# Kernel tuning notes

Hardware: AMD Instinct MI355X
Metric: run time of the kernel (lower is better)

The kernel has to match this reference:

```python
import jax, jax.numpy as jnp
import numpy as np

NUM_LEVELS = 16
FEATS_PER_LEVEL = 2
LOG2_HASHMAP = 19
TABLE_SIZE = 1 << LOG2_HASHMAP
BASE_RES = 16
DESIRED_RES = 4096
PER_LEVEL_SCALE = float(np.exp(np.log(DESIRED_RES / BASE_RES) / (NUM_LEVELS - 1)))
PRIMES = (np.uint32(1), np.uint32(2654435761), np.uint32(805459861))
N_POINTS = 2_000_000


def _level_features(x, table, level):
    # x: [N,3] in [0,1]; table: [TABLE_SIZE, F]
    scale = BASE_RES * (PER_LEVEL_SCALE ** level) - 1.0
    res = int(np.ceil(scale)) + 1
    dense = (res ** 3) <= TABLE_SIZE  # tcnn uses dense indexing when grid fits
    pos = x * scale + 0.5
    pos0 = jnp.floor(pos)
    w = pos - pos0                     # trilinear weights, [N,3]
    base = pos0.astype(jnp.uint32)
    out = jnp.zeros((x.shape[0], table.shape[1]), dtype=table.dtype)
    for c in range(8):                 # 8 corners of the voxel
        offs = [(c >> d) & 1 for d in range(3)]
        pc = [jnp.minimum(base[:, d] + np.uint32(offs[d]), np.uint32(res - 1)) for d in range(3)]
        if dense:
            idx = pc[0] + pc[1] * np.uint32(res) + pc[2] * np.uint32(res * res)
        else:
            idx = (pc[0] * PRIMES[0]) ^ (pc[1] * PRIMES[1]) ^ (pc[2] * PRIMES[2])
            idx = idx & np.uint32(TABLE_SIZE - 1)
        wt = jnp.ones(x.shape[0], dtype=x.dtype)
        for d in range(3):
            wt = wt * (w[:, d] if offs[d] else (1.0 - w[:, d]))
        out = out + wt[:, None] * table[idx.astype(jnp.int32)]
    return out


def hashgrid_encode(x, tables):
    # x: [N,3] in [0,1]; tables: [L, TABLE_SIZE, F] -> [N, L*F]
    return jnp.concatenate(
        [_level_features(x, tables[l], l) for l in range(NUM_LEVELS)], axis=-1)


def setup_inputs() -> dict:
    key = jax.random.key(0)
    k1, k2, k3, k4, k5 = jax.random.split(key, 5)
    points = jax.random.uniform(k1, (N_POINTS, 3), dtype=jnp.float32)
    # tcnn hashgrid init: uniform(-1e-4, 1e-4)
    tables = jax.random.uniform(k2, (NUM_LEVELS, TABLE_SIZE, FEATS_PER_LEVEL),
                                minval=-1e-4, maxval=1e-4, dtype=jnp.float32)
    def kaiming(k, fan_out, fan_in):
        bound = np.sqrt(2.0) * np.sqrt(3.0 / fan_in)
        return jax.random.uniform(k, (fan_out, fan_in), minval=-bound, maxval=bound,
                                  dtype=jnp.float32)
    W1 = kaiming(k3, 32, 32)
    W2 = kaiming(k4, 32, 32)
    W3 = kaiming(k5, 4, 32)
    aabb = jnp.stack([jnp.zeros(3, jnp.float32), jnp.ones(3, jnp.float32)])
    return {"points": points, "tables": tables, "W1": W1, "W2": W2, "W3": W3,
            "aabb": aabb}


def reference(points, tables, W1, W2, W3, aabb):
    texc = jnp.clip((points - aabb[0][None, :]) / (aabb[1] - aabb[0])[None, :], 0.0, 1.0)
    enc = hashgrid_encode(texc, tables)            # [N, 32]
    h = jax.nn.relu(enc @ W1.T)
    h = jax.nn.relu(h @ W2.T)
    out = h @ W3.T                                 # [N, 4]
    mn = jnp.array([0.0, 0.0, 0.0, 0.01], dtype=out.dtype)
    mx = jnp.array([1.0, 1.0, 1.0, 1.0], dtype=out.dtype)
    return jax.nn.sigmoid(out) * (mx - mn) + mn
```

## Files before the change

### kernel.cpp

```cpp
#include <hip/hip_runtime.h>
#include <cmath>


namespace {
constexpr int kLevels = 16;
constexpr unsigned kTableSize = 1u << 19;
constexpr unsigned kMask = kTableSize - 1u;
constexpr int kCells = 32768;

typedef _Float16 half2_t __attribute__((ext_vector_type(2)));
typedef unsigned int u32;

struct LevelParams {
  float scale[kLevels];
  unsigned res[kLevels];
  int dense[kLevels];
  unsigned toff[kLevels];
  unsigned cnt[kLevels];
};
}

__global__ __launch_bounds__(256)
void conv_tables_kernel(const float2* __restrict__ src, u32* __restrict__ dst,
                        LevelParams lp,
                        const float* __restrict__ W1, const float* __restrict__ W2,
                        const float* __restrict__ W3, half2_t* __restrict__ Wh)
{
  int gid = blockIdx.x * blockDim.x + threadIdx.x;
  if (gid < 512) {
    Wh[gid] = half2_t{(_Float16)W1[2 * gid], (_Float16)W1[2 * gid + 1]};
  } else if (gid < 1024) {
    int t = gid - 512;
    Wh[512 + t] = half2_t{(_Float16)W2[2 * t], (_Float16)W2[2 * t + 1]};
  } else if (gid < 1088) {
    int t = gid - 1024;
    Wh[1024 + t] = half2_t{(_Float16)W3[2 * t], (_Float16)W3[2 * t + 1]};
  }
  int l = blockIdx.x >> 11;
  unsigned e = (unsigned)((blockIdx.x & 2047) * blockDim.x + threadIdx.x);
  if (l < kLevels && e < lp.cnt[l]) {
    float2 v = src[(size_t)l * kTableSize + e];
    dst[lp.toff[l] + e] =
        __builtin_bit_cast(u32, half2_t{(_Float16)v.x, (_Float16)v.y});
  }
}

__device__ __forceinline__ void texc_of(const float* __restrict__ pts,
                                        const float* __restrict__ aabb, int i,
                                        float& x, float& y, float& z)
{
  float a0x = aabb[0], a0y = aabb[1], a0z = aabb[2];
  float a1x = aabb[3], a1y = aabb[4], a1z = aabb[5];
  x = fminf(fmaxf((pts[3 * i + 0] - a0x) / (a1x - a0x), 0.f), 1.f);
  y = fminf(fmaxf((pts[3 * i + 1] - a0y) / (a1y - a0y), 0.f), 1.f);
  z = fminf(fmaxf((pts[3 * i + 2] - a0z) / (a1z - a0z), 0.f), 1.f);
}

__device__ __forceinline__ int cell_of(float x, float y, float z)
{
  int cx = min((int)(x * 32.f), 31);
  int cy = min((int)(y * 32.f), 31);
  int cz = min((int)(z * 32.f), 31);
  return cx + (cy << 5) + (cz << 10);
}

__global__ __launch_bounds__(256)
void zero_hist_kernel(u32* __restrict__ hist)
{
  int i = blockIdx.x * blockDim.x + threadIdx.x;
  if (i < kCells) hist[i] = 0u;
}

__global__ __launch_bounds__(256)
void hist_kernel(const float* __restrict__ points, const float* __restrict__ aabb,
                 u32* __restrict__ hist, int n)
{
  int i = blockIdx.x * blockDim.x + threadIdx.x;
  if (i >= n) return;
  float x, y, z;
  texc_of(points, aabb, i, x, y, z);
  atomicAdd(&hist[cell_of(x, y, z)], 1u);
}

__global__ __launch_bounds__(1024)
void scan_kernel(u32* __restrict__ hist)
{
  __shared__ u32 sm[1024];
  int t = threadIdx.x;
  u32 loc[32];
  u32 s = 0;
  #pragma unroll
  for (int k = 0; k < 32; ++k) { loc[k] = hist[t * 32 + k]; s += loc[k]; }
  sm[t] = s;
  __syncthreads();
  u32 v = s;
  for (int off = 1; off < 1024; off <<= 1) {
    u32 a = (t >= off) ? sm[t - off] : 0u;
    __syncthreads();
    v += a;
    sm[t] = v;
    __syncthreads();
  }
  u32 run = v - s;
  #pragma unroll
  for (int k = 0; k < 32; ++k) { hist[t * 32 + k] = run; run += loc[k]; }
}

__global__ __launch_bounds__(256)
void scatter_kernel(const float* __restrict__ points, const float* __restrict__ aabb,
                    u32* __restrict__ cstart, float4* __restrict__ sorted,
                    u32* __restrict__ perm, int n)
{
  int i = blockIdx.x * blockDim.x + threadIdx.x;
  if (i >= n) return;
  float x, y, z;
  texc_of(points, aabb, i, x, y, z);
  int c = cell_of(x, y, z);
  u32 slot = atomicAdd(&cstart[c], 1u);
  sorted[slot] = float4{x, y, z, 0.f};
  perm[slot] = (u32)i;
}

__device__ __forceinline__ u32 sel4(uint4 v, u32 j) {
  u32 lo = (j & 1u) ? v.y : v.x;
  u32 hi = (j & 1u) ? v.w : v.z;
  return (j & 2u) ? hi : lo;
}

__global__ __launch_bounds__(256)
void encode_kernel(const float4* __restrict__ pts,
                   const u32* __restrict__ tables,
                   half2_t* __restrict__ enc,
                   LevelParams lp, int n, int bpl)
{
  int l = blockIdx.x / bpl;
  int i = (blockIdx.x - l * bpl) * blockDim.x + threadIdx.x;
  if (i >= n) return;

  float4 p = pts[i];
  float x = p.x, y = p.y, z = p.z;

  float s = lp.scale[l];
  unsigned res = lp.res[l];
  bool dense = (lp.dense[l] != 0);
  unsigned rm1 = res - 1u;
  unsigned res2 = res * res;
  const u32* tab = tables + lp.toff[l];

  float fx = x * s + 0.5f, fy = y * s + 0.5f, fz = z * s + 0.5f;
  float fx0 = floorf(fx), fy0 = floorf(fy), fz0 = floorf(fz);
  float wx = fx - fx0, wy = fy - fy0, wz = fz - fz0;
  unsigned bx = (unsigned)fx0, by = (unsigned)fy0, bz = (unsigned)fz0;

  unsigned pcx0 = min(bx, rm1), pcx1 = min(bx + 1u, rm1);

  u32 idx0[4], idx1[4];
  #pragma unroll
  for (int q = 0; q < 4; ++q) {
    unsigned oy = (unsigned)(q & 1);
    unsigned oz = (unsigned)(q >> 1);
    unsigned pcy = min(by + oy, rm1);
    unsigned pcz = min(bz + oz, rm1);
    if (dense) {
      u32 b = pcy * res + pcz * res2;
      idx0[q] = pcx0 + b;
      idx1[q] = pcx1 + b;
    } else {
      u32 h = (pcy * 2654435761u) ^ (pcz * 805459861u);
      idx0[q] = (pcx0 ^ h) & kMask;
      idx1[q] = (pcx1 ^ h) & kMask;
    }
  }

  uint4 v[4];
  #pragma unroll
  for (int q = 0; q < 4; ++q)
    v[q] = *reinterpret_cast<const uint4*>(tab + (idx0[q] & ~3u));

  u32 e1x[4] = {0u, 0u, 0u, 0u};
  #pragma unroll
  for (int q = 0; q < 4; ++q) {
    if ((idx0[q] ^ idx1[q]) >= 4u) e1x[q] = tab[idx1[q]];
  }

  float wx1 = wx, wx0 = 1.f - wx;
  float acc0 = 0.f, acc1 = 0.f;
  #pragma unroll
  for (int q = 0; q < 4; ++q) {
    unsigned oy = (unsigned)(q & 1);
    unsigned oz = (unsigned)(q >> 1);
    float wyz = (oy ? wy : 1.f - wy) * (oz ? wz : 1.f - wz);
    u32 e0 = sel4(v[q], idx0[q] & 3u);
    u32 e1g = sel4(v[q], idx1[q] & 3u);
    u32 e1 = ((idx0[q] ^ idx1[q]) < 4u) ? e1g : e1x[q];
    half2_t f0 = __builtin_bit_cast(half2_t, e0);
    half2_t f1 = __builtin_bit_cast(half2_t, e1);
    float w0 = wyz * wx0, w1 = wyz * wx1;
    acc0 += w0 * (float)f0.x + w1 * (float)f1.x;
    acc1 += w0 * (float)f0.y + w1 * (float)f1.y;
  }
  enc[(size_t)l * n + i] = half2_t{(_Float16)acc0, (_Float16)acc1};
}

__global__ __launch_bounds__(256)
void encode_raw_kernel(const float* __restrict__ points,
                       const u32* __restrict__ tables,
                       const float* __restrict__ aabb,
                       half2_t* __restrict__ enc,
                       LevelParams lp, int n, int bpl)
{
  int l = blockIdx.x / bpl;
  int i = (blockIdx.x - l * bpl) * blockDim.x + threadIdx.x;
  if (i >= n) return;
  float x, y, z;
  texc_of(points, aabb, i, x, y, z);

  float s = lp.scale[l];
  unsigned res = lp.res[l];
  bool dense = (lp.dense[l] != 0);
  unsigned rm1 = res - 1u;
  unsigned res2 = res * res;
  const u32* tab = tables + lp.toff[l];

  float fx = x * s + 0.5f, fy = y * s + 0.5f, fz = z * s + 0.5f;
  float fx0 = floorf(fx), fy0 = floorf(fy), fz0 = floorf(fz);
  float wx = fx - fx0, wy = fy - fy0, wz = fz - fz0;
  unsigned bx = (unsigned)fx0, by = (unsigned)fy0, bz = (unsigned)fz0;
  unsigned pcx0 = min(bx, rm1), pcx1 = min(bx + 1u, rm1);

  u32 idx0[4], idx1[4];
  #pragma unroll
  for (int q = 0; q < 4; ++q) {
    unsigned oy = (unsigned)(q & 1);
    unsigned oz = (unsigned)(q >> 1);
    unsigned pcy = min(by + oy, rm1);
    unsigned pcz = min(bz + oz, rm1);
    if (dense) {
      u32 b = pcy * res + pcz * res2;
      idx0[q] = pcx0 + b;
      idx1[q] = pcx1 + b;
    } else {
      u32 h = (pcy * 2654435761u) ^ (pcz * 805459861u);
      idx0[q] = (pcx0 ^ h) & kMask;
      idx1[q] = (pcx1 ^ h) & kMask;
    }
  }
  uint4 v[4];
  #pragma unroll
  for (int q = 0; q < 4; ++q)
    v[q] = *reinterpret_cast<const uint4*>(tab + (idx0[q] & ~3u));
  u32 e1x[4] = {0u, 0u, 0u, 0u};
  #pragma unroll
  for (int q = 0; q < 4; ++q) {
    if ((idx0[q] ^ idx1[q]) >= 4u) e1x[q] = tab[idx1[q]];
  }
  float wx1 = wx, wx0 = 1.f - wx;
  float acc0 = 0.f, acc1 = 0.f;
  #pragma unroll
  for (int q = 0; q < 4; ++q) {
    unsigned oy = (unsigned)(q & 1);
    unsigned oz = (unsigned)(q >> 1);
    float wyz = (oy ? wy : 1.f - wy) * (oz ? wz : 1.f - wz);
    u32 e0 = sel4(v[q], idx0[q] & 3u);
    u32 e1g = sel4(v[q], idx1[q] & 3u);
    u32 e1 = ((idx0[q] ^ idx1[q]) < 4u) ? e1g : e1x[q];
    half2_t f0 = __builtin_bit_cast(half2_t, e0);
    half2_t f1 = __builtin_bit_cast(half2_t, e1);
    float w0 = wyz * wx0, w1 = wyz * wx1;
    acc0 += w0 * (float)f0.x + w1 * (float)f1.x;
    acc1 += w0 * (float)f0.y + w1 * (float)f1.y;
  }
  enc[(size_t)l * n + i] = half2_t{(_Float16)acc0, (_Float16)acc1};
}

__device__ __forceinline__ float dot2_acc(half2_t a, half2_t b, float c) {
#if __has_builtin(__builtin_amdgcn_fdot2)
  return __builtin_amdgcn_fdot2(a, b, c, false);
#else
  return c + (float)a.x * (float)b.x + (float)a.y * (float)b.y;
#endif
}

__global__ __launch_bounds__(256)
void mlp_kernel(const half2_t* __restrict__ enc,
                const half2_t* __restrict__ Wh,
                const u32* __restrict__ perm,
                float* __restrict__ out, int n)
{
  int i = blockIdx.x * blockDim.x + threadIdx.x;
  if (i >= n) return;

  u32 orig = perm ? perm[i] : (u32)i;

  half2_t e[16];
  #pragma unroll
  for (int l = 0; l < kLevels; ++l) e[l] = enc[(size_t)l * n + i];

  const half2_t* W1h = Wh;
  const half2_t* W2h = Wh + 512;
  const half2_t* W3h = Wh + 1024;

  float h1f[32];
  #pragma unroll
  for (int j = 0; j < 32; ++j) {
    float acc = 0.f;
    #pragma unroll
    for (int k = 0; k < 16; ++k) acc = dot2_acc(e[k], W1h[16 * j + k], acc);
    h1f[j] = fmaxf(acc, 0.f);
  }
  half2_t h1[16];
  #pragma unroll
  for (int k = 0; k < 16; ++k)
    h1[k] = half2_t{(_Float16)h1f[2 * k], (_Float16)h1f[2 * k + 1]};

  float h2f[32];
  #pragma unroll
  for (int j = 0; j < 32; ++j) {
    float acc = 0.f;
    #pragma unroll
    for (int k = 0; k < 16; ++k) acc = dot2_acc(h1[k], W2h[16 * j + k], acc);
    h2f[j] = fmaxf(acc, 0.f);
  }
  half2_t h2[16];
  #pragma unroll
  for (int k = 0; k < 16; ++k)
    h2[k] = half2_t{(_Float16)h2f[2 * k], (_Float16)h2f[2 * k + 1]};

  float o[4];
  #pragma unroll
  for (int j = 0; j < 4; ++j) {
    float acc = 0.f;
    #pragma unroll
    for (int k = 0; k < 16; ++k) acc = dot2_acc(h2[k], W3h[16 * j + k], acc);
    o[j] = acc;
  }

  float4 r;
  r.x = 1.f / (1.f + __expf(-o[0]));
  r.y = 1.f / (1.f + __expf(-o[1]));
  r.z = 1.f / (1.f + __expf(-o[2]));
  r.w = 0.99f / (1.f + __expf(-o[3])) + 0.01f;
  reinterpret_cast<float4*>(out)[orig] = r;
}

__global__ __launch_bounds__(256)
void hashgrid_mlp_kernel(const float* __restrict__ points,
                         const float* __restrict__ tables,
                         const float* __restrict__ W1,
                         const float* __restrict__ W2,
                         const float* __restrict__ W3,
                         const float* __restrict__ aabb,
                         float* __restrict__ out,
                         LevelParams lp, int n)
{
  int i = blockIdx.x * blockDim.x + threadIdx.x;
  if (i >= n) return;
  float x, y, z;
  texc_of(points, aabb, i, x, y, z);
  float enc[2 * kLevels];
  #pragma unroll
  for (int l = 0; l < kLevels; ++l) {
    float s = lp.scale[l];
    unsigned res = lp.res[l];
    bool dense = (lp.dense[l] != 0);
    unsigned rm1 = res - 1u;
    unsigned res2 = res * res;
    float fx = x * s + 0.5f, fy = y * s + 0.5f, fz = z * s + 0.5f;
    float fx0 = floorf(fx), fy0 = floorf(fy), fz0 = floorf(fz);
    float wx = fx - fx0, wy = fy - fy0, wz = fz - fz0;
    unsigned bx = (unsigned)fx0, by = (unsigned)fy0, bz = (unsigned)fz0;
    const float2* tab = reinterpret_cast<const float2*>(tables) + (size_t)l * kTableSize;
    float acc0 = 0.f, acc1 = 0.f;
    #pragma unroll
    for (int c = 0; c < 8; ++c) {
      unsigned ox = (unsigned)(c & 1);
      unsigned oy = (unsigned)((c >> 1) & 1);
      unsigned oz = (unsigned)((c >> 2) & 1);
      unsigned pcx = min(bx + ox, rm1);
      unsigned pcy = min(by + oy, rm1);
      unsigned pcz = min(bz + oz, rm1);
      unsigned idx;
      if (dense) idx = pcx + pcy * res + pcz * res2;
      else idx = (pcx ^ (pcy * 2654435761u) ^ (pcz * 805459861u)) & kMask;
      float wt = (ox ? wx : 1.f - wx) * (oy ? wy : 1.f - wy) * (oz ? wz : 1.f - wz);
      float2 f = tab[idx];
      acc0 += wt * f.x;
      acc1 += wt * f.y;
    }
    enc[2 * l + 0] = acc0;
    enc[2 * l + 1] = acc1;
  }
  float h1[32];
  #pragma unroll
  for (int j = 0; j < 32; ++j) {
    float acc = 0.f;
    #pragma unroll
    for (int k = 0; k < 32; ++k) acc += enc[k] * W1[32 * j + k];
    h1[j] = fmaxf(acc, 0.f);
  }
  float h2[32];
  #pragma unroll
  for (int j = 0; j < 32; ++j) {
    float acc = 0.f;
    #pragma unroll
    for (int k = 0; k < 32; ++k) acc += h1[k] * W2[32 * j + k];
    h2[j] = fmaxf(acc, 0.f);
  }
  float o[4];
  #pragma unroll
  for (int j = 0; j < 4; ++j) {
    float acc = 0.f;
    #pragma unroll
    for (int k = 0; k < 32; ++k) acc += h2[k] * W3[32 * j + k];
    o[j] = acc;
  }
  float4 r;
  r.x = 1.f / (1.f + __expf(-o[0]));
  r.y = 1.f / (1.f + __expf(-o[1]));
  r.z = 1.f / (1.f + __expf(-o[2]));
  r.w = 0.99f / (1.f + __expf(-o[3])) + 0.01f;
  reinterpret_cast<float4*>(out)[i] = r;
}

extern "C" void kernel_launch(void* const* d_in, const int* in_sizes, int n_in,
                              void* d_out, int out_size, void* d_ws, size_t ws_size,
                              hipStream_t stream) {
  const float* points = (const float*)d_in[0];
  const float* tables = (const float*)d_in[1];
  const float* W1     = (const float*)d_in[2];
  const float* W2     = (const float*)d_in[3];
  const float* W3     = (const float*)d_in[4];
  const float* aabb   = (const float*)d_in[5];
  float* out = (float*)d_out;
  int n = in_sizes[0] / 3;

  LevelParams lp;
  const double pls = std::exp(std::log(4096.0 / 16.0) / 15.0);
  unsigned off = 0;
  for (int l = 0; l < kLevels; ++l) {
    double s = 16.0 * std::pow(pls, (double)l) - 1.0;
    lp.scale[l] = (float)s;
    long long res = (long long)std::ceil(s) + 1;
    lp.res[l] = (unsigned)res;
    long long r3 = res * res * res;
    lp.dense[l] = (r3 <= (long long)kTableSize) ? 1 : 0;
    lp.cnt[l] = lp.dense[l] ? (unsigned)r3 : kTableSize;
    lp.toff[l] = off;
    off += (lp.cnt[l] + 3u) & ~3u;
  }

  const int block = 256;
  const size_t tab_f16_bytes = (size_t)off * sizeof(u32);
  const size_t enc_bytes     = (size_t)kLevels * (size_t)n * sizeof(half2_t);
  const size_t perm_bytes    = (size_t)n * sizeof(u32);
  const size_t hist_bytes    = (size_t)kCells * sizeof(u32);
  const size_t w_bytes       = 1088 * sizeof(half2_t);

  const size_t need_sorted = tab_f16_bytes + enc_bytes + perm_bytes + hist_bytes + w_bytes;
  const size_t need_raw    = tab_f16_bytes + enc_bytes + w_bytes;
  const bool out_fits_sorted = (size_t)out_size >= (size_t)4 * (size_t)n;

  const int grid_n = (n + block - 1) / block;
  const int bpl = grid_n;

  if (ws_size >= need_sorted && out_fits_sorted) {
    char* p = (char*)d_ws;
    u32*     tab_f16 = (u32*)p;                   p += tab_f16_bytes;
    half2_t* enc     = (half2_t*)p;               p += enc_bytes;
    u32*     perm    = (u32*)p;                   p += perm_bytes;
    u32*     hist    = (u32*)p;                   p += hist_bytes;
    half2_t* Wh      = (half2_t*)p;
    float4*  sorted  = (float4*)d_out;

    conv_tables_kernel<<<kLevels * 2048, block, 0, stream>>>(
        reinterpret_cast<const float2*>(tables), tab_f16, lp, W1, W2, W3, Wh);
    zero_hist_kernel<<<(kCells + block - 1) / block, block, 0, stream>>>(hist);
    hist_kernel<<<grid_n, block, 0, stream>>>(points, aabb, hist, n);
    scan_kernel<<<1, 1024, 0, stream>>>(hist);
    scatter_kernel<<<grid_n, block, 0, stream>>>(points, aabb, hist, sorted, perm, n);
    encode_kernel<<<bpl * kLevels, block, 0, stream>>>(
        sorted, tab_f16, enc, lp, n, bpl);
    mlp_kernel<<<grid_n, block, 0, stream>>>(enc, Wh, perm, out, n);
  } else if (ws_size >= need_raw) {
    char* p = (char*)d_ws;
    u32*     tab_f16 = (u32*)p;                   p += tab_f16_bytes;
    half2_t* enc     = (half2_t*)p;               p += enc_bytes;
    half2_t* Wh      = (half2_t*)p;

    conv_tables_kernel<<<kLevels * 2048, block, 0, stream>>>(
        reinterpret_cast<const float2*>(tables), tab_f16, lp, W1, W2, W3, Wh);
    encode_raw_kernel<<<bpl * kLevels, block, 0, stream>>>(
        points, tab_f16, aabb, enc, lp, n, bpl);
    mlp_kernel<<<grid_n, block, 0, stream>>>(enc, Wh, nullptr, out, n);
  } else {
    hashgrid_mlp_kernel<<<grid_n, block, 0, stream>>>(
        points, tables, W1, W2, W3, aabb, out, lp, n);
  }
}
```

Before: 850.5 us.

## Refine spatial binning to 64^3 cells with multi-block scan, alias histogram into enc buffer

Raises the counting-sort grid from 32^3 to 64^3 cells so points sorted into each cell are spatially tighter, which should improve cache locality of hash-table gathers in the encode kernel. The single-block scan is replaced by a two-stage scan (per-block scan plus a block-totals scan), and scatter adds the block base to the per-cell offset. Histogram zeroing is folded into the table conversion kernel, and the histogram is aliased into the enc workspace, which is overwritten later. This adds an extra kernel launch and makes the finer-grid histogram and scatter atomics less contended but more spread out.

```diff
diff --git a/kernel.cpp b/kernel.cpp
--- a/kernel.cpp
+++ b/kernel.cpp
@@ -6,7 +6,8 @@
 constexpr int kLevels = 16;
 constexpr unsigned kTableSize = 1u << 19;
 constexpr unsigned kMask = kTableSize - 1u;
-constexpr int kCells = 32768;
+constexpr int kCells = 262144;
+constexpr int kScanBlocks = 256;
 
 typedef _Float16 half2_t __attribute__((ext_vector_type(2)));
 typedef unsigned int u32;
@@ -24,7 +25,8 @@
 void conv_tables_kernel(const float2* __restrict__ src, u32* __restrict__ dst,
                         LevelParams lp,
                         const float* __restrict__ W1, const float* __restrict__ W2,
-                        const float* __restrict__ W3, half2_t* __restrict__ Wh)
+                        const float* __restrict__ W3, half2_t* __restrict__ Wh,
+                        u32* __restrict__ hist0)
 {
   int gid = blockIdx.x * blockDim.x + threadIdx.x;
   if (gid < 512) {
@@ -36,6 +38,7 @@
     int t = gid - 1024;
     Wh[1024 + t] = half2_t{(_Float16)W3[2 * t], (_Float16)W3[2 * t + 1]};
   }
+  if (hist0 && gid < kCells) hist0[gid] = 0u;
   int l = blockIdx.x >> 11;
   unsigned e = (unsigned)((blockIdx.x & 2047) * blockDim.x + threadIdx.x);
   if (l < kLevels && e < lp.cnt[l]) {
@@ -58,17 +61,10 @@
 
 __device__ __forceinline__ int cell_of(float x, float y, float z)
 {
-  int cx = min((int)(x * 32.f), 31);
-  int cy = min((int)(y * 32.f), 31);
-  int cz = min((int)(z * 32.f), 31);
-  return cx + (cy << 5) + (cz << 10);
-}
-
-__global__ __launch_bounds__(256)
-void zero_hist_kernel(u32* __restrict__ hist)
-{
-  int i = blockIdx.x * blockDim.x + threadIdx.x;
-  if (i < kCells) hist[i] = 0u;
+  int cx = min((int)(x * 64.f), 63);
+  int cy = min((int)(y * 64.f), 63);
+  int cz = min((int)(z * 64.f), 63);
+  return cx + (cy << 6) + (cz << 12);
 }
 
 __global__ __launch_bounds__(256)
@@ -83,17 +79,15 @@
 }
 
 __global__ __launch_bounds__(1024)
-void scan_kernel(u32* __restrict__ hist)
+void scanA_kernel(u32* __restrict__ hist, u32* __restrict__ btot)
 {
   __shared__ u32 sm[1024];
   int t = threadIdx.x;
-  u32 loc[32];
-  u32 s = 0;
-  #pragma unroll
-  for (int k = 0; k < 32; ++k) { loc[k] = hist[t * 32 + k]; s += loc[k]; }
-  sm[t] = s;
+  int i = (blockIdx.x << 10) + t;
+  u32 x = hist[i];
+  sm[t] = x;
   __syncthreads();
-  u32 v = s;
+  u32 v = x;
   for (int off = 1; off < 1024; off <<= 1) {
     u32 a = (t >= off) ? sm[t - off] : 0u;
     __syncthreads();
@@ -101,22 +95,40 @@
     sm[t] = v;
     __syncthreads();
   }
-  u32 run = v - s;
-  #pragma unroll
-  for (int k = 0; k < 32; ++k) { hist[t * 32 + k] = run; run += loc[k]; }
+  hist[i] = v - x;
+  if (t == 1023) btot[blockIdx.x] = v;
+}
+
+__global__ __launch_bounds__(256)
+void scanB_kernel(const u32* __restrict__ btot, u32* __restrict__ bbase)
+{
+  __shared__ u32 sm[256];
+  int t = threadIdx.x;
+  u32 x = btot[t];
+  sm[t] = x;
+  __syncthreads();
+  u32 v = x;
+  for (int off = 1; off < 256; off <<= 1) {
+    u32 a = (t >= off) ? sm[t - off] : 0u;
+    __syncthreads();
+    v += a;
+    sm[t] = v;
+    __syncthreads();
+  }
+  bbase[t] = v - x;
 }
 
 __global__ __launch_bounds__(256)
 void scatter_kernel(const float* __restrict__ points, const float* __restrict__ aabb,
-                    u32* __restrict__ cstart, float4* __restrict__ sorted,
-                    u32* __restrict__ perm, int n)
+                    u32* __restrict__ hist, const u32* __restrict__ bbase,
+                    float4* __restrict__ sorted, u32* __restrict__ perm, int n)
 {
   int i = blockIdx.x * blockDim.x + threadIdx.x;
   if (i >= n) return;
   float x, y, z;
   texc_of(points, aabb, i, x, y, z);
   int c = cell_of(x, y, z);
-  u32 slot = atomicAdd(&cstart[c], 1u);
+  u32 slot = bbase[c >> 10] + atomicAdd(&hist[c], 1u);
   sorted[slot] = float4{x, y, z, 0.f};
   perm[slot] = (u32)i;
 }
@@ -453,31 +465,34 @@
   const size_t tab_f16_bytes = (size_t)off * sizeof(u32);
   const size_t enc_bytes     = (size_t)kLevels * (size_t)n * sizeof(half2_t);
   const size_t perm_bytes    = (size_t)n * sizeof(u32);
-  const size_t hist_bytes    = (size_t)kCells * sizeof(u32);
   const size_t w_bytes       = 1088 * sizeof(half2_t);
 
-  const size_t need_sorted = tab_f16_bytes + enc_bytes + perm_bytes + hist_bytes + w_bytes;
+  const size_t need_sorted = tab_f16_bytes + enc_bytes + perm_bytes + w_bytes;
   const size_t need_raw    = tab_f16_bytes + enc_bytes + w_bytes;
   const bool out_fits_sorted = (size_t)out_size >= (size_t)4 * (size_t)n;
+  const bool enc_fits_hist = enc_bytes >= (size_t)(kCells + 512) * sizeof(u32);
 
   const int grid_n = (n + block - 1) / block;
   const int bpl = grid_n;
 
-  if (ws_size >= need_sorted && out_fits_sorted) {
+  if (ws_size >= need_sorted && out_fits_sorted && enc_fits_hist) {
     char* p = (char*)d_ws;
     u32*     tab_f16 = (u32*)p;                   p += tab_f16_bytes;
     half2_t* enc     = (half2_t*)p;               p += enc_bytes;
     u32*     perm    = (u32*)p;                   p += perm_bytes;
-    u32*     hist    = (u32*)p;                   p += hist_bytes;
     half2_t* Wh      = (half2_t*)p;
+    u32*     hist    = (u32*)enc;
+    u32*     btot    = hist + kCells;
+    u32*     bbase   = btot + kScanBlocks;
     float4*  sorted  = (float4*)d_out;
 
     conv_tables_kernel<<<kLevels * 2048, block, 0, stream>>>(
-        reinterpret_cast<const float2*>(tables), tab_f16, lp, W1, W2, W3, Wh);
-    zero_hist_kernel<<<(kCells + block - 1) / block, block, 0, stream>>>(hist);
+        reinterpret_cast<const float2*>(tables), tab_f16, lp, W1, W2, W3, Wh, hist);
     hist_kernel<<<grid_n, block, 0, stream>>>(points, aabb, hist, n);
-    scan_kernel<<<1, 1024, 0, stream>>>(hist);
-    scatter_kernel<<<grid_n, block, 0, stream>>>(points, aabb, hist, sorted, perm, n);
+    scanA_kernel<<<kScanBlocks, 1024, 0, stream>>>(hist, btot);
+    scanB_kernel<<<1, 256, 0, stream>>>(btot, bbase);
+    scatter_kernel<<<grid_n, block, 0, stream>>>(points, aabb, hist, bbase,
+                                                 sorted, perm, n);
     encode_kernel<<<bpl * kLevels, block, 0, stream>>>(
         sorted, tab_f16, enc, lp, n, bpl);
     mlp_kernel<<<grid_n, block, 0, stream>>>(enc, Wh, perm, out, n);
@@ -488,7 +503,8 @@
     half2_t* Wh      = (half2_t*)p;
 
     conv_tables_kernel<<<kLevels * 2048, block, 0, stream>>>(
-        reinterpret_cast<const float2*>(tables), tab_f16, lp, W1, W2, W3, Wh);
+        reinterpret_cast<const float2*>(tables), tab_f16, lp, W1, W2, W3, Wh,
+        nullptr);
     encode_raw_kernel<<<bpl * kLevels, block, 0, stream>>>(
         points, tab_f16, aabb, enc, lp, n, bpl);
     mlp_kernel<<<grid_n, block, 0, stream>>>(enc, Wh, nullptr, out, n);
```

New measurement: 799.7 us. 6.0% less time.
